# Optimization experiments

Hardware: AMD Instinct MI355X
Metric: run time of the kernel (lower is better)

## Reference

```python
import jax, jax.numpy as jnp
import numpy as np

B, D, H, S = 32768, 512, 8, 3  # batch, stream_dim, heads, num_streams
DH = D // H
EPS = 1e-5


def setup_inputs() -> dict:
    key = jax.random.key(0)
    ks = jax.random.split(key, 16)
    sc = lambda fan_in: 1.0 / np.sqrt(fan_in)
    return {
        "kinematic_h": jax.random.normal(ks[0], (B, D), jnp.float32),
        "color_h": jax.random.normal(ks[1], (B, D), jnp.float32),
        "spinor_h": jax.random.normal(ks[2], (B, D), jnp.float32),
        # MultiheadAttention packed in-proj and out-proj
        "w_in": jax.random.normal(ks[3], (3 * D, D), jnp.float32) * sc(D),
        "b_in": jnp.zeros((3 * D,), jnp.float32),
        "w_out": jax.random.normal(ks[4], (D, D), jnp.float32) * sc(D),
        "b_out": jnp.zeros((D,), jnp.float32),
        # stream gate: Linear(3D -> 3) + softmax
        "w_gate": jax.random.normal(ks[5], (S, S * D), jnp.float32) * sc(S * D),
        "b_gate": jnp.zeros((S,), jnp.float32),
        # fusion MLP: Linear(3D -> 2D), SiLU, Linear(2D -> D)
        "w1": jax.random.normal(ks[6], (2 * D, S * D), jnp.float32) * sc(S * D),
        "b1": jnp.zeros((2 * D,), jnp.float32),
        "w2": jax.random.normal(ks[7], (D, 2 * D), jnp.float32) * sc(2 * D),
        "b2": jnp.zeros((D,), jnp.float32),
        # LayerNorm
        "gamma": jnp.ones((D,), jnp.float32),
        "beta": jnp.zeros((D,), jnp.float32),
    }


def reference(kinematic_h, color_h, spinor_h, w_in, b_in, w_out, b_out,
              w_gate, b_gate, w1, b1, w2, b2, gamma, beta):
    stacked = jnp.stack([kinematic_h, color_h, spinor_h], axis=1)  # [B,S,D]
    b = stacked.shape[0]
    # self-attention (Q=K=V=stacked), packed QKV projection
    qkv = stacked @ w_in.T + b_in  # [B,S,3D]
    q, k, v = jnp.split(qkv, 3, axis=-1)
    q = q.reshape(b, S, H, DH)
    k = k.reshape(b, S, H, DH)
    v = v.reshape(b, S, H, DH)
    scores = jnp.einsum("bqhd,bkhd->bhqk", q, k) / np.sqrt(DH)
    attn = jax.nn.softmax(scores, axis=-1)
    out = jnp.einsum("bhqk,bkhd->bqhd", attn, v).reshape(b, S, D)
    attn_out = stacked + (out @ w_out.T + b_out)  # residual, [B,S,D]
    # gating softmax over streams
    flat = attn_out.reshape(b, S * D)
    gates = jax.nn.softmax(flat @ w_gate.T + b_gate, axis=-1)[..., None]  # [B,S,1]
    gated = (attn_out * gates).reshape(b, S * D)
    # fusion MLP (dropout=eval no-op)
    h = jax.nn.silu(gated @ w1.T + b1)
    fused = h @ w2.T + b2  # [B,D]
    # LayerNorm
    mu = jnp.mean(fused, axis=-1, keepdims=True)
    var = jnp.var(fused, axis=-1, keepdims=True)
    return (fused - mu) * jax.lax.rsqrt(var + EPS) * gamma + beta
```

## Files before the change

kernel.cpp:

```cpp
#include <hip/hip_runtime.h>
#include <stdint.h>


typedef float f32x4 __attribute__((ext_vector_type(4)));
typedef short bf16x8 __attribute__((ext_vector_type(8)));

__device__ __forceinline__ float bf2f(unsigned short h) {
  return __uint_as_float(((unsigned)h) << 16);
}
__device__ __forceinline__ unsigned short f2bf(float f) {
  unsigned u = __float_as_uint(f);
  u += 0x7FFFu + ((u >> 16) & 1u);
  return (unsigned short)(u >> 16);
}
__device__ __forceinline__ ushort4 f2bf4(float4 v) {
  return make_ushort4(f2bf(v.x), f2bf(v.y), f2bf(v.z), f2bf(v.w));
}

__device__ __forceinline__ void async_cp16(const void* g, void* lds) {
  __builtin_amdgcn_global_load_lds(
      (const __attribute__((address_space(1))) void*)g,
      (__attribute__((address_space(3))) void*)lds, 16, 0, 0);
}

__global__ void __launch_bounds__(256) cvtbf(const float4* __restrict__ src,
                                             ushort4* __restrict__ dst, int n4) {
  int i = blockIdx.x * 256 + threadIdx.x;
  if (i < n4) dst[i] = f2bf4(src[i]);
}

__global__ void __launch_bounds__(256) pack3(const float4* __restrict__ X0,
                                             const float4* __restrict__ X1,
                                             const float4* __restrict__ X2,
                                             ushort4* __restrict__ S) {
  int tid = blockIdx.x * 256 + threadIdx.x;
  int b = tid >> 7, c = tid & 127;
  long base = (long)(3 * b) * 128 + c;
  S[base]       = f2bf4(X0[tid]);
  S[base + 128] = f2bf4(X1[tid]);
  S[base + 256] = f2bf4(X2[tid]);
}

__global__ void __launch_bounds__(256)
qkv_attn(const unsigned short* __restrict__ S,
         const unsigned short* __restrict__ Wi,
         const float* __restrict__ bin,
         unsigned short* __restrict__ AO) {
  __shared__ unsigned short lds[96 * 200];
  unsigned short* Abuf = lds;
  unsigned short* Bbuf = lds + 6144;

  const int t = threadIdx.x;
  const int lane = t & 63;
  const int wave = t >> 6;
  const int wm = wave >> 1, wn = wave & 1;

  const int ny = gridDim.y;
  const int id = blockIdx.y * 8 + blockIdx.x;
  const int xcd = id & 7, j = id >> 3;
  const int h = j & 7;
  const long m0 = (long)(xcd * (ny >> 3) + (j >> 3)) * 96;

  const int trow = t >> 3;
  const int swz = ((t & 7) ^ (trow & 7)) << 3;
  const unsigned short* Ag = S + (m0 + trow) * 512 + swz;
  const unsigned short* Bg = Wi + ((long)h * 64 + trow) * 512 + swz;
  unsigned short* AsD = Abuf + t * 8;
  unsigned short* BsD = Bbuf + t * 8;

  f32x4 acc[3][6] = {};
  const int arow0 = wm * 48 + (lane & 15);
  const int brow0 = wn * 96 + (lane & 15);

  for (int k0 = 0; k0 < 512; k0 += 64) {
    __syncthreads();
#pragma unroll
    for (int r = 0; r < 3; r++)
      async_cp16(Ag + (long)r * 32 * 512 + k0, AsD + r * 2048);
#pragma unroll
    for (int r = 0; r < 6; r++)
      async_cp16(Bg + (long)((r >> 1) * 512 + (r & 1) * 32) * 512 + k0, BsD + r * 2048);
    __syncthreads();
#pragma unroll
    for (int kk = 0; kk < 2; kk++) {
      const int sc = ((kk * 4 + (lane >> 4)) ^ (lane & 7)) << 3;
      bf16x8 af[3], bfr[6];
#pragma unroll
      for (int mt = 0; mt < 3; mt++)
        af[mt] = *(const bf16x8*)&Abuf[(arow0 + mt * 16) * 64 + sc];
#pragma unroll
      for (int nt = 0; nt < 6; nt++)
        bfr[nt] = *(const bf16x8*)&Bbuf[(brow0 + nt * 16) * 64 + sc];
#pragma unroll
      for (int mt = 0; mt < 3; mt++)
#pragma unroll
        for (int nt = 0; nt < 6; nt++)
          acc[mt][nt] = __builtin_amdgcn_mfma_f32_16x16x32_bf16(
              af[mt], bfr[nt], acc[mt][nt], 0, 0, 0);
    }
  }

  __syncthreads();
  const int crow0 = wm * 48 + ((lane >> 4) << 2);
  const int ccol0 = wn * 96 + (lane & 15);
#pragma unroll
  for (int nt = 0; nt < 6; nt++) {
    const int col = ccol0 + nt * 16;
    const float bv = bin[(col >> 6) * 512 + h * 64 + (col & 63)];
#pragma unroll
    for (int mt = 0; mt < 3; mt++)
#pragma unroll
      for (int r = 0; r < 4; r++)
        lds[(crow0 + mt * 16 + r) * 200 + col] = f2bf(acc[mt][nt][r] + bv);
  }
  __syncthreads();

  const int bi = lane >> 3;
  const int l8 = lane & 7;
  const int r0 = (wave * 8 + bi) * 3;
  float q[3][8], k[3][8], v[3][8];
#pragma unroll
  for (int s = 0; s < 3; s++) {
    const unsigned short* rowp = &lds[(r0 + s) * 200 + l8 * 8];
    uint4 qu = *(const uint4*)(rowp);
    uint4 ku = *(const uint4*)(rowp + 64);
    uint4 vu = *(const uint4*)(rowp + 128);
    const unsigned* qw = (const unsigned*)&qu;
    const unsigned* kw = (const unsigned*)&ku;
    const unsigned* vw = (const unsigned*)&vu;
#pragma unroll
    for (int jj = 0; jj < 4; jj++) {
      q[s][2 * jj]     = __uint_as_float(qw[jj] << 16);
      q[s][2 * jj + 1] = __uint_as_float(qw[jj] & 0xffff0000u);
      k[s][2 * jj]     = __uint_as_float(kw[jj] << 16);
      k[s][2 * jj + 1] = __uint_as_float(kw[jj] & 0xffff0000u);
      v[s][2 * jj]     = __uint_as_float(vw[jj] << 16);
      v[s][2 * jj + 1] = __uint_as_float(vw[jj] & 0xffff0000u);
    }
  }
  float p[3][3];
#pragma unroll
  for (int s = 0; s < 3; s++)
#pragma unroll
    for (int u = 0; u < 3; u++) {
      float d = 0.f;
#pragma unroll
      for (int e = 0; e < 8; e++) d = fmaf(q[s][e], k[u][e], d);
      p[s][u] = d;
    }
#pragma unroll
  for (int m = 1; m < 8; m <<= 1)
#pragma unroll
    for (int s = 0; s < 3; s++)
#pragma unroll
      for (int u = 0; u < 3; u++) p[s][u] += __shfl_xor(p[s][u], m, 64);

  unsigned short* ob = AO + (m0 + r0) * 512 + h * 64 + l8 * 8;
#pragma unroll
  for (int s = 0; s < 3; s++) {
    float a0 = p[s][0] * 0.125f, a1 = p[s][1] * 0.125f, a2 = p[s][2] * 0.125f;
    float mx = fmaxf(a0, fmaxf(a1, a2));
    float e0 = __expf(a0 - mx), e1 = __expf(a1 - mx), e2 = __expf(a2 - mx);
    float inv = 1.0f / (e0 + e1 + e2);
    unsigned ow[4];
#pragma unroll
    for (int jj = 0; jj < 4; jj++) {
      float lo = (e0 * v[0][2 * jj] + e1 * v[1][2 * jj] + e2 * v[2][2 * jj]) * inv;
      float hi = (e0 * v[0][2 * jj + 1] + e1 * v[1][2 * jj + 1] + e2 * v[2][2 * jj + 1]) * inv;
      ow[jj] = (unsigned)f2bf(lo) | ((unsigned)f2bf(hi) << 16);
    }
    *(uint4*)(ob + s * 512) = *(uint4*)ow;
  }
}

enum { EPI_BF16 = 0, EPI_RES = 1, EPI_SILU = 2, EPI_F32 = 3 };

template <int EPI>
__global__ void __launch_bounds__(512, 2)
gemm256(const unsigned short* __restrict__ A,
        const unsigned short* __restrict__ W,
        const float* __restrict__ bias,
        const unsigned short* __restrict__ Res,
        void* __restrict__ Out,
        int K, int N) {
  __shared__ unsigned short As[2][16384];
  __shared__ unsigned short Bs[2][16384];
  const int t = threadIdx.x;
  const int lane = t & 63;
  const int wave = t >> 6;
  const int wm = wave >> 2, wn = wave & 3;

  const int nb = gridDim.x;
  const int nblocks = nb * gridDim.y;
  const int id = blockIdx.y * nb + blockIdx.x;
  const int lid = ((nblocks & 7) == 0) ? ((id & 7) * (nblocks >> 3) + (id >> 3)) : id;
  const long bm = (long)(lid / nb) * 256;
  const long bn = (long)(lid % nb) * 256;

  const int srow = t >> 3;
  const int sch = ((t & 7) ^ (srow & 7)) << 3;
  const unsigned short* Ag = A + (bm + srow) * (long)K + sch;
  const unsigned short* Wg = W + (bn + srow) * (long)K + sch;

  const int NT = K >> 6;

  f32x4 acc[8][4] = {};
  const int arow = wm * 128 + (lane & 15);
  const int brow = wn * 64 + (lane & 15);

#define STGA(buf, q, k0) \
  async_cp16(Ag + (long)((q) * 64) * K + (k0), &As[buf][(q) * 4096 + t * 8])
#define STGB(buf, q, k0) \
  async_cp16(Wg + (long)((q) * 64) * K + (k0), &Bs[buf][(q) * 4096 + t * 8])

  STGA(0, 0, 0); STGA(0, 2, 0);
  STGB(0, 0, 0); STGB(0, 1, 0); STGB(0, 2, 0); STGB(0, 3, 0);
  STGA(0, 1, 0); STGA(0, 3, 0);
  if (NT > 1) { STGA(1, 0, 64); STGA(1, 2, 64); }
  asm volatile("s_waitcnt vmcnt(0)" ::: "memory");
  __builtin_amdgcn_s_barrier();

  for (int tt = 0; tt < NT; ++tt) {
    const unsigned short* Ab = As[tt & 1];
    const unsigned short* Bb = Bs[tt & 1];
    const int nbuf = (tt & 1) ^ 1;
    const int k1 = (tt + 1) << 6, k2 = (tt + 2) << 6;
    const bool s1 = (tt + 1 < NT), s2 = (tt + 2 < NT);
    bf16x8 af[4], bfv[4];

    {
      const int sc = ((lane >> 4) ^ (lane & 7)) << 3;
#pragma unroll
      for (int i = 0; i < 4; ++i)
        af[i] = *(const bf16x8*)&Ab[(arow + i * 16) * 64 + sc];
#pragma unroll
      for (int i = 0; i < 4; ++i)
        bfv[i] = *(const bf16x8*)&Bb[(brow + i * 16) * 64 + sc];
      if (s1) { STGB(nbuf, 0, k1); STGB(nbuf, 1, k1); }
      __builtin_amdgcn_s_barrier();
      asm volatile("s_waitcnt lgkmcnt(0)" ::: "memory");
      __builtin_amdgcn_s_setprio(1);
#pragma unroll
      for (int mi = 0; mi < 4; ++mi)
#pragma unroll
        for (int ni = 0; ni < 4; ++ni)
          acc[mi][ni] = __builtin_amdgcn_mfma_f32_16x16x32_bf16(
              af[mi], bfv[ni], acc[mi][ni], 0, 0, 0);
      __builtin_amdgcn_s_setprio(0);
      asm volatile("s_waitcnt vmcnt(4)" ::: "memory");
      __builtin_amdgcn_s_barrier();
    }
    {
      const int sc = ((lane >> 4) ^ (lane & 7)) << 3;
#pragma unroll
      for (int i = 0; i < 4; ++i)
        af[i] = *(const bf16x8*)&Ab[(arow + (4 + i) * 16) * 64 + sc];
      if (s1) { STGB(nbuf, 2, k1); STGB(nbuf, 3, k1); }
      __builtin_amdgcn_s_barrier();
      asm volatile("s_waitcnt lgkmcnt(0)" ::: "memory");
      __builtin_amdgcn_s_setprio(1);
#pragma unroll
      for (int mi = 0; mi < 4; ++mi)
#pragma unroll
        for (int ni = 0; ni < 4; ++ni)
          acc[4 + mi][ni] = __builtin_amdgcn_mfma_f32_16x16x32_bf16(
              af[mi], bfv[ni], acc[4 + mi][ni], 0, 0, 0);
      __builtin_amdgcn_s_setprio(0);
      __builtin_amdgcn_s_barrier();
    }
    {
      const int sc = ((4 + (lane >> 4)) ^ (lane & 7)) << 3;
#pragma unroll
      for (int i = 0; i < 4; ++i)
        af[i] = *(const bf16x8*)&Ab[(arow + i * 16) * 64 + sc];
#pragma unroll
      for (int i = 0; i < 4; ++i)
        bfv[i] = *(const bf16x8*)&Bb[(brow + i * 16) * 64 + sc];
      if (s1) { STGA(nbuf, 1, k1); STGA(nbuf, 3, k1); }
      __builtin_amdgcn_s_barrier();
      asm volatile("s_waitcnt lgkmcnt(0)" ::: "memory");
      __builtin_amdgcn_s_setprio(1);
#pragma unroll
      for (int mi = 0; mi < 4; ++mi)
#pragma unroll
        for (int ni = 0; ni < 4; ++ni)
          acc[mi][ni] = __builtin_amdgcn_mfma_f32_16x16x32_bf16(
              af[mi], bfv[ni], acc[mi][ni], 0, 0, 0);
      __builtin_amdgcn_s_setprio(0);
      __builtin_amdgcn_s_barrier();
    }
    {
      const int sc = ((4 + (lane >> 4)) ^ (lane & 7)) << 3;
#pragma unroll
      for (int i = 0; i < 4; ++i)
        af[i] = *(const bf16x8*)&Ab[(arow + (4 + i) * 16) * 64 + sc];
      if (s2) { STGA(tt & 1, 0, k2); STGA(tt & 1, 2, k2); }
      __builtin_amdgcn_s_barrier();
      asm volatile("s_waitcnt lgkmcnt(0)" ::: "memory");
      __builtin_amdgcn_s_setprio(1);
#pragma unroll
      for (int mi = 0; mi < 4; ++mi)
#pragma unroll
        for (int ni = 0; ni < 4; ++ni)
          acc[4 + mi][ni] = __builtin_amdgcn_mfma_f32_16x16x32_bf16(
              af[mi], bfv[ni], acc[4 + mi][ni], 0, 0, 0);
      __builtin_amdgcn_s_setprio(0);
      asm volatile("s_waitcnt vmcnt(4)" ::: "memory");
      __builtin_amdgcn_s_barrier();
    }
  }
#undef STGA
#undef STGB

  const long row0 = bm + wm * 128 + ((lane >> 4) << 2);
  const int col0 = (int)bn + wn * 64 + (lane & 15);
#pragma unroll
  for (int nt = 0; nt < 4; ++nt) {
    const int col = col0 + nt * 16;
    const float bv = bias[col];
#pragma unroll
    for (int mt = 0; mt < 8; ++mt) {
      const long rbase = row0 + mt * 16;
#pragma unroll
      for (int r = 0; r < 4; ++r) {
        float v = acc[mt][nt][r] + bv;
        const long idx = (rbase + r) * (long)N + col;
        if (EPI == EPI_RES) v += bf2f(Res[idx]);
        if (EPI == EPI_SILU) v = v * (1.0f / (1.0f + __expf(-v)));
        if (EPI == EPI_F32)
          ((float*)Out)[idx] = v;
        else
          ((unsigned short*)Out)[idx] = f2bf(v);
      }
    }
  }
}

__global__ void __launch_bounds__(256) gate3(const unsigned short* AT,
                                             const float* __restrict__ WG,
                                             const float* __restrict__ BG,
                                             unsigned short* G) {
  int row = blockIdx.x * 4 + (threadIdx.x >> 6);
  int lane = threadIdx.x & 63;
  const unsigned short* rp = AT + (long)row * 1536 + lane * 8;
  float x[3][8];
  float p[3] = {0.f, 0.f, 0.f};
#pragma unroll
  for (int seg = 0; seg < 3; seg++) {
    uint4 u = *(const uint4*)(rp + seg * 512);
    const unsigned* uw = (const unsigned*)&u;
#pragma unroll
    for (int j = 0; j < 4; j++) {
      x[seg][2 * j]     = __uint_as_float(uw[j] << 16);
      x[seg][2 * j + 1] = __uint_as_float(uw[j] & 0xffff0000u);
    }
    const int e0 = seg * 512 + lane * 8;
#pragma unroll
    for (int g = 0; g < 3; g++) {
      const float* wp = WG + g * 1536 + e0;
#pragma unroll
      for (int e = 0; e < 8; e++) p[g] = fmaf(x[seg][e], wp[e], p[g]);
    }
  }
#pragma unroll
  for (int m = 1; m < 64; m <<= 1)
#pragma unroll
    for (int g = 0; g < 3; g++) p[g] += __shfl_xor(p[g], m, 64);
  float g0 = p[0] + BG[0], g1 = p[1] + BG[1], g2 = p[2] + BG[2];
  float mx = fmaxf(g0, fmaxf(g1, g2));
  g0 = __expf(g0 - mx); g1 = __expf(g1 - mx); g2 = __expf(g2 - mx);
  float inv = 1.0f / (g0 + g1 + g2);
  float gs[3] = {g0 * inv, g1 * inv, g2 * inv};
  unsigned short* op = G + (long)row * 1536 + lane * 8;
#pragma unroll
  for (int seg = 0; seg < 3; seg++) {
    unsigned ow[4];
#pragma unroll
    for (int j = 0; j < 4; j++)
      ow[j] = (unsigned)f2bf(x[seg][2 * j] * gs[seg]) |
              ((unsigned)f2bf(x[seg][2 * j + 1] * gs[seg]) << 16);
    *(uint4*)(op + seg * 512) = *(uint4*)ow;
  }
}

__global__ void __launch_bounds__(256) lnorm(const float* __restrict__ F,
                                             const float* __restrict__ gamma,
                                             const float* __restrict__ beta,
                                             float* __restrict__ out) {
  int row = blockIdx.x * 4 + (threadIdx.x >> 6);
  int lane = threadIdx.x & 63;
  const float4* fr = (const float4*)(F + (long)row * 512);
  float4 a = fr[lane], c = fr[lane + 64];
  float s = a.x + a.y + a.z + a.w + c.x + c.y + c.z + c.w;
  float ss = a.x * a.x + a.y * a.y + a.z * a.z + a.w * a.w +
             c.x * c.x + c.y * c.y + c.z * c.z + c.w * c.w;
#pragma unroll
  for (int m = 1; m < 64; m <<= 1) {
    s += __shfl_xor(s, m, 64);
    ss += __shfl_xor(ss, m, 64);
  }
  float mean = s * (1.0f / 512.0f);
  float var = ss * (1.0f / 512.0f) - mean * mean;
  float rstd = rsqrtf(var + 1e-5f);
  const float4* g4 = (const float4*)gamma;
  const float4* b4 = (const float4*)beta;
  float4 g0 = g4[lane], g1 = g4[lane + 64], be0 = b4[lane], be1 = b4[lane + 64];
  float4 o0, o1;
  o0.x = (a.x - mean) * rstd * g0.x + be0.x;
  o0.y = (a.y - mean) * rstd * g0.y + be0.y;
  o0.z = (a.z - mean) * rstd * g0.z + be0.z;
  o0.w = (a.w - mean) * rstd * g0.w + be0.w;
  o1.x = (c.x - mean) * rstd * g1.x + be1.x;
  o1.y = (c.y - mean) * rstd * g1.y + be1.y;
  o1.z = (c.z - mean) * rstd * g1.z + be1.z;
  o1.w = (c.w - mean) * rstd * g1.w + be1.w;
  float4* orow = (float4*)(out + (long)row * 512);
  orow[lane] = o0;
  orow[lane + 64] = o1;
}

extern "C" void kernel_launch(void* const* d_in, const int* in_sizes, int n_in,
                              void* d_out, int out_size, void* d_ws, size_t ws_size,
                              hipStream_t stream) {
  const float* kin    = (const float*)d_in[0];
  const float* colr   = (const float*)d_in[1];
  const float* spi    = (const float*)d_in[2];
  const float* w_in   = (const float*)d_in[3];
  const float* b_in   = (const float*)d_in[4];
  const float* w_out  = (const float*)d_in[5];
  const float* b_out  = (const float*)d_in[6];
  const float* w_gate = (const float*)d_in[7];
  const float* b_gate = (const float*)d_in[8];
  const float* w1     = (const float*)d_in[9];
  const float* b1     = (const float*)d_in[10];
  const float* w2     = (const float*)d_in[11];
  const float* b2     = (const float*)d_in[12];
  const float* gamma  = (const float*)d_in[13];
  const float* beta   = (const float*)d_in[14];
  float* out = (float*)d_out;

  long Bc = 32768;
  while (Bc > 1024 && (size_t)(6291456 + 9216 * Bc) > ws_size) Bc >>= 1;
  const int nch = (int)(32768 / Bc);

  char* ws = (char*)d_ws;
  unsigned short* Wic = (unsigned short*)(ws);
  unsigned short* Woc = (unsigned short*)(ws + 1572864);
  unsigned short* W1c = (unsigned short*)(ws + 2097152);
  unsigned short* W2c = (unsigned short*)(ws + 5242880);
  char* Sb  = ws + 6291456;
  char* AOb = Sb + 3072 * Bc;
  char* ATb = AOb + 3072 * Bc;

  cvtbf<<<768, 256, 0, stream>>>((const float4*)w_in, (ushort4*)Wic, 196608);
  cvtbf<<<256, 256, 0, stream>>>((const float4*)w_out, (ushort4*)Woc, 65536);
  cvtbf<<<1536, 256, 0, stream>>>((const float4*)w1, (ushort4*)W1c, 393216);
  cvtbf<<<512, 256, 0, stream>>>((const float4*)w2, (ushort4*)W2c, 131072);

  for (int c = 0; c < nch; c++) {
    const long boff = (long)c * Bc;
    unsigned short* S_c  = (unsigned short*)Sb;
    unsigned short* AO_c = (unsigned short*)AOb;
    unsigned short* AT_c = (unsigned short*)ATb;
    unsigned short* G_c  = AT_c;
    unsigned short* H_c  = (unsigned short*)AOb;
    float*          F_c  = (float*)Sb;

    pack3<<<(int)(Bc / 2), 256, 0, stream>>>(
        (const float4*)(kin + boff * 512), (const float4*)(colr + boff * 512),
        (const float4*)(spi + boff * 512), (ushort4*)S_c);
    qkv_attn<<<dim3(8, (int)(Bc / 32)), 256, 0, stream>>>(S_c, Wic, b_in, AO_c);
    gemm256<EPI_RES><<<dim3(2, (int)(3 * Bc / 256)), 512, 0, stream>>>(
        AO_c, Woc, b_out, S_c, AT_c, 512, 512);
    gate3<<<(int)(Bc / 4), 256, 0, stream>>>(AT_c, w_gate, b_gate, G_c);
    gemm256<EPI_SILU><<<dim3(4, (int)(Bc / 256)), 512, 0, stream>>>(
        G_c, W1c, b1, nullptr, H_c, 1536, 1024);
    gemm256<EPI_F32><<<dim3(2, (int)(Bc / 256)), 512, 0, stream>>>(
        H_c, W2c, b2, nullptr, F_c, 1024, 512);
    lnorm<<<(int)(Bc / 4), 256, 0, stream>>>(F_c, gamma, beta, out + boff * 512);
  }
}
```

Baseline: 841.6 us.

## Replace pipelined 256x256 GEMM with simple 128x128 single-buffer GEMM, packed bf16 converts

Swaps the hand-scheduled double-buffered 256x256-tile GEMM (512 threads, prefetch interleaved with MFMA phases, setprio) for a simpler 128x128-tile kernel with 256 threads, a single LDS buffer and barriers around each K step. The grids are rescaled to match. Separately, the bf16 conversion helpers now use the HIP packed float2-to-bf16x2 intrinsic in every kernel. The smaller tile gives more blocks and lower LDS and register use, but it loses load/compute overlap and halves operand reuse per tile, so the GEMMs may become latency-bound.

```diff
diff --git a/kernel.cpp b/kernel.cpp
--- a/kernel.cpp
+++ b/kernel.cpp
@@ -1,4 +1,5 @@
 #include <hip/hip_runtime.h>
+#include <hip/hip_bf16.h>
 #include <stdint.h>
 
 
@@ -9,12 +10,15 @@
   return __uint_as_float(((unsigned)h) << 16);
 }
 __device__ __forceinline__ unsigned short f2bf(float f) {
-  unsigned u = __float_as_uint(f);
-  u += 0x7FFFu + ((u >> 16) & 1u);
-  return (unsigned short)(u >> 16);
-}
-__device__ __forceinline__ ushort4 f2bf4(float4 v) {
-  return make_ushort4(f2bf(v.x), f2bf(v.y), f2bf(v.z), f2bf(v.w));
+  __hip_bfloat16 h = __float2bfloat16(f);
+  return *reinterpret_cast<unsigned short*>(&h);
+}
+__device__ __forceinline__ unsigned pack2bf(float lo, float hi) {
+  __hip_bfloat162 h2 = __float22bfloat162_rn(make_float2(lo, hi));
+  return *reinterpret_cast<unsigned*>(&h2);
+}
+__device__ __forceinline__ uint2 f2bf4p(float4 v) {
+  return make_uint2(pack2bf(v.x, v.y), pack2bf(v.z, v.w));
 }
 
 __device__ __forceinline__ void async_cp16(const void* g, void* lds) {
@@ -24,21 +28,21 @@
 }
 
 __global__ void __launch_bounds__(256) cvtbf(const float4* __restrict__ src,
-                                             ushort4* __restrict__ dst, int n4) {
+                                             uint2* __restrict__ dst, int n4) {
   int i = blockIdx.x * 256 + threadIdx.x;
-  if (i < n4) dst[i] = f2bf4(src[i]);
+  if (i < n4) dst[i] = f2bf4p(src[i]);
 }
 
 __global__ void __launch_bounds__(256) pack3(const float4* __restrict__ X0,
                                              const float4* __restrict__ X1,
                                              const float4* __restrict__ X2,
-                                             ushort4* __restrict__ S) {
+                                             uint2* __restrict__ S) {
   int tid = blockIdx.x * 256 + threadIdx.x;
   int b = tid >> 7, c = tid & 127;
   long base = (long)(3 * b) * 128 + c;
-  S[base]       = f2bf4(X0[tid]);
-  S[base + 128] = f2bf4(X1[tid]);
-  S[base + 256] = f2bf4(X2[tid]);
+  S[base]       = f2bf4p(X0[tid]);
+  S[base + 128] = f2bf4p(X1[tid]);
+  S[base + 256] = f2bf4p(X2[tid]);
 }
 
 __global__ void __launch_bounds__(256)
@@ -108,10 +112,15 @@
     const int col = ccol0 + nt * 16;
     const float bv = bin[(col >> 6) * 512 + h * 64 + (col & 63)];
 #pragma unroll
-    for (int mt = 0; mt < 3; mt++)
-#pragma unroll
-      for (int r = 0; r < 4; r++)
-        lds[(crow0 + mt * 16 + r) * 200 + col] = f2bf(acc[mt][nt][r] + bv);
+    for (int mt = 0; mt < 3; mt++) {
+      const int rb = (crow0 + mt * 16) * 200 + col;
+      const unsigned p01 = pack2bf(acc[mt][nt][0] + bv, acc[mt][nt][1] + bv);
+      const unsigned p23 = pack2bf(acc[mt][nt][2] + bv, acc[mt][nt][3] + bv);
+      lds[rb]       = (unsigned short)p01;
+      lds[rb + 200] = (unsigned short)(p01 >> 16);
+      lds[rb + 400] = (unsigned short)p23;
+      lds[rb + 600] = (unsigned short)(p23 >> 16);
+    }
   }
   __syncthreads();
 
@@ -167,7 +176,7 @@
     for (int jj = 0; jj < 4; jj++) {
       float lo = (e0 * v[0][2 * jj] + e1 * v[1][2 * jj] + e2 * v[2][2 * jj]) * inv;
       float hi = (e0 * v[0][2 * jj + 1] + e1 * v[1][2 * jj + 1] + e2 * v[2][2 * jj + 1]) * inv;
-      ow[jj] = (unsigned)f2bf(lo) | ((unsigned)f2bf(hi) << 16);
+      ow[jj] = pack2bf(lo, hi);
     }
     *(uint4*)(ob + s * 512) = *(uint4*)ow;
   }
@@ -176,153 +185,76 @@
 enum { EPI_BF16 = 0, EPI_RES = 1, EPI_SILU = 2, EPI_F32 = 3 };
 
 template <int EPI>
-__global__ void __launch_bounds__(512, 2)
-gemm256(const unsigned short* __restrict__ A,
+__global__ void __launch_bounds__(256)
+gemm_bt(const unsigned short* __restrict__ A,
         const unsigned short* __restrict__ W,
         const float* __restrict__ bias,
         const unsigned short* __restrict__ Res,
         void* __restrict__ Out,
         int K, int N) {
-  __shared__ unsigned short As[2][16384];
-  __shared__ unsigned short Bs[2][16384];
+  __shared__ unsigned short As[128 * 64];
+  __shared__ unsigned short Bs[128 * 64];
   const int t = threadIdx.x;
   const int lane = t & 63;
   const int wave = t >> 6;
-  const int wm = wave >> 2, wn = wave & 3;
+  const int wm = wave >> 1, wn = wave & 1;
 
   const int nb = gridDim.x;
   const int nblocks = nb * gridDim.y;
   const int id = blockIdx.y * nb + blockIdx.x;
   const int lid = ((nblocks & 7) == 0) ? ((id & 7) * (nblocks >> 3) + (id >> 3)) : id;
-  const long bm = (long)(lid / nb) * 256;
-  const long bn = (long)(lid % nb) * 256;
+  const long bm = (long)(lid / nb) * 128;
+  const long bn = (long)(lid % nb) * 128;
 
   const int srow = t >> 3;
-  const int sch = ((t & 7) ^ (srow & 7)) << 3;
-  const unsigned short* Ag = A + (bm + srow) * (long)K + sch;
-  const unsigned short* Wg = W + (bn + srow) * (long)K + sch;
-
-  const int NT = K >> 6;
-
-  f32x4 acc[8][4] = {};
-  const int arow = wm * 128 + (lane & 15);
-  const int brow = wn * 64 + (lane & 15);
-
-#define STGA(buf, q, k0) \
-  async_cp16(Ag + (long)((q) * 64) * K + (k0), &As[buf][(q) * 4096 + t * 8])
-#define STGB(buf, q, k0) \
-  async_cp16(Wg + (long)((q) * 64) * K + (k0), &Bs[buf][(q) * 4096 + t * 8])
-
-  STGA(0, 0, 0); STGA(0, 2, 0);
-  STGB(0, 0, 0); STGB(0, 1, 0); STGB(0, 2, 0); STGB(0, 3, 0);
-  STGA(0, 1, 0); STGA(0, 3, 0);
-  if (NT > 1) { STGA(1, 0, 64); STGA(1, 2, 64); }
-  asm volatile("s_waitcnt vmcnt(0)" ::: "memory");
-  __builtin_amdgcn_s_barrier();
-
-  for (int tt = 0; tt < NT; ++tt) {
-    const unsigned short* Ab = As[tt & 1];
-    const unsigned short* Bb = Bs[tt & 1];
-    const int nbuf = (tt & 1) ^ 1;
-    const int k1 = (tt + 1) << 6, k2 = (tt + 2) << 6;
-    const bool s1 = (tt + 1 < NT), s2 = (tt + 2 < NT);
-    bf16x8 af[4], bfv[4];
-
-    {
-      const int sc = ((lane >> 4) ^ (lane & 7)) << 3;
-#pragma unroll
-      for (int i = 0; i < 4; ++i)
-        af[i] = *(const bf16x8*)&Ab[(arow + i * 16) * 64 + sc];
-#pragma unroll
-      for (int i = 0; i < 4; ++i)
-        bfv[i] = *(const bf16x8*)&Bb[(brow + i * 16) * 64 + sc];
-      if (s1) { STGB(nbuf, 0, k1); STGB(nbuf, 1, k1); }
-      __builtin_amdgcn_s_barrier();
-      asm volatile("s_waitcnt lgkmcnt(0)" ::: "memory");
-      __builtin_amdgcn_s_setprio(1);
-#pragma unroll
-      for (int mi = 0; mi < 4; ++mi)
-#pragma unroll
-        for (int ni = 0; ni < 4; ++ni)
-          acc[mi][ni] = __builtin_amdgcn_mfma_f32_16x16x32_bf16(
-              af[mi], bfv[ni], acc[mi][ni], 0, 0, 0);
-      __builtin_amdgcn_s_setprio(0);
-      asm volatile("s_waitcnt vmcnt(4)" ::: "memory");
-      __builtin_amdgcn_s_barrier();
-    }
-    {
-      const int sc = ((lane >> 4) ^ (lane & 7)) << 3;
-#pragma unroll
-      for (int i = 0; i < 4; ++i)
-        af[i] = *(const bf16x8*)&Ab[(arow + (4 + i) * 16) * 64 + sc];
-      if (s1) { STGB(nbuf, 2, k1); STGB(nbuf, 3, k1); }
-      __builtin_amdgcn_s_barrier();
-      asm volatile("s_waitcnt lgkmcnt(0)" ::: "memory");
-      __builtin_amdgcn_s_setprio(1);
-#pragma unroll
-      for (int mi = 0; mi < 4; ++mi)
-#pragma unroll
-        for (int ni = 0; ni < 4; ++ni)
-          acc[4 + mi][ni] = __builtin_amdgcn_mfma_f32_16x16x32_bf16(
-              af[mi], bfv[ni], acc[4 + mi][ni], 0, 0, 0);
-      __builtin_amdgcn_s_setprio(0);
-      __builtin_amdgcn_s_barrier();
-    }
-    {
-      const int sc = ((4 + (lane >> 4)) ^ (lane & 7)) << 3;
-#pragma unroll
-      for (int i = 0; i < 4; ++i)
-        af[i] = *(const bf16x8*)&Ab[(arow + i * 16) * 64 + sc];
-#pragma unroll
-      for (int i = 0; i < 4; ++i)
-        bfv[i] = *(const bf16x8*)&Bb[(brow + i * 16) * 64 + sc];
-      if (s1) { STGA(nbuf, 1, k1); STGA(nbuf, 3, k1); }
-      __builtin_amdgcn_s_barrier();
-      asm volatile("s_waitcnt lgkmcnt(0)" ::: "memory");
-      __builtin_amdgcn_s_setprio(1);
-#pragma unroll
-      for (int mi = 0; mi < 4; ++mi)
-#pragma unroll
-        for (int ni = 0; ni < 4; ++ni)
-          acc[mi][ni] = __builtin_amdgcn_mfma_f32_16x16x32_bf16(
-              af[mi], bfv[ni], acc[mi][ni], 0, 0, 0);
-      __builtin_amdgcn_s_setprio(0);
-      __builtin_amdgcn_s_barrier();
-    }
-    {
-      const int sc = ((4 + (lane >> 4)) ^ (lane & 7)) << 3;
-#pragma unroll
-      for (int i = 0; i < 4; ++i)
-        af[i] = *(const bf16x8*)&Ab[(arow + (4 + i) * 16) * 64 + sc];
-      if (s2) { STGA(tt & 1, 0, k2); STGA(tt & 1, 2, k2); }
-      __builtin_amdgcn_s_barrier();
-      asm volatile("s_waitcnt lgkmcnt(0)" ::: "memory");
-      __builtin_amdgcn_s_setprio(1);
-#pragma unroll
-      for (int mi = 0; mi < 4; ++mi)
-#pragma unroll
-        for (int ni = 0; ni < 4; ++ni)
-          acc[4 + mi][ni] = __builtin_amdgcn_mfma_f32_16x16x32_bf16(
-              af[mi], bfv[ni], acc[4 + mi][ni], 0, 0, 0);
-      __builtin_amdgcn_s_setprio(0);
-      asm volatile("s_waitcnt vmcnt(4)" ::: "memory");
-      __builtin_amdgcn_s_barrier();
-    }
-  }
-#undef STGA
-#undef STGB
-
-  const long row0 = bm + wm * 128 + ((lane >> 4) << 2);
+  const int schunk = ((t & 7) ^ (srow & 7)) << 3;
+  const unsigned short* Ag = A + (bm + srow) * (long)K + schunk;
+  const unsigned short* Wg = W + (bn + srow) * (long)K + schunk;
+  unsigned short* AsD = As + t * 8;
+  unsigned short* BsD = Bs + t * 8;
+
+  f32x4 acc[4][4] = {};
+  const int arow0 = wm * 64 + (lane & 15);
+  const int brow0 = wn * 64 + (lane & 15);
+
+  for (int k0 = 0; k0 < K; k0 += 64) {
+    __syncthreads();
+#pragma unroll
+    for (int i = 0; i < 4; i++) {
+      async_cp16(Ag + (long)(i * 32) * K + k0, AsD + i * 2048);
+      async_cp16(Wg + (long)(i * 32) * K + k0, BsD + i * 2048);
+    }
+    __syncthreads();
+#pragma unroll
+    for (int kk = 0; kk < 2; kk++) {
+      const int sc = ((kk * 4 + (lane >> 4)) ^ (lane & 7)) << 3;
+      bf16x8 af[4], bfr[4];
+#pragma unroll
+      for (int mt = 0; mt < 4; mt++)
+        af[mt] = *(const bf16x8*)&As[(arow0 + mt * 16) * 64 + sc];
+#pragma unroll
+      for (int nt = 0; nt < 4; nt++)
+        bfr[nt] = *(const bf16x8*)&Bs[(brow0 + nt * 16) * 64 + sc];
+#pragma unroll
+      for (int mt = 0; mt < 4; mt++)
+#pragma unroll
+        for (int nt = 0; nt < 4; nt++)
+          acc[mt][nt] = __builtin_amdgcn_mfma_f32_16x16x32_bf16(
+              af[mt], bfr[nt], acc[mt][nt], 0, 0, 0);
+    }
+  }
+
+  const long row0 = bm + wm * 64 + ((lane >> 4) << 2);
   const int col0 = (int)bn + wn * 64 + (lane & 15);
 #pragma unroll
-  for (int nt = 0; nt < 4; ++nt) {
+  for (int nt = 0; nt < 4; nt++) {
     const int col = col0 + nt * 16;
     const float bv = bias[col];
 #pragma unroll
-    for (int mt = 0; mt < 8; ++mt) {
+    for (int mt = 0; mt < 4; mt++) {
       const long rbase = row0 + mt * 16;
 #pragma unroll
-      for (int r = 0; r < 4; ++r) {
+      for (int r = 0; r < 4; r++) {
         float v = acc[mt][nt][r] + bv;
         const long idx = (rbase + r) * (long)N + col;
         if (EPI == EPI_RES) v += bf2f(Res[idx]);
@@ -377,8 +309,7 @@
     unsigned ow[4];
 #pragma unroll
     for (int j = 0; j < 4; j++)
-      ow[j] = (unsigned)f2bf(x[seg][2 * j] * gs[seg]) |
-              ((unsigned)f2bf(x[seg][2 * j + 1] * gs[seg]) << 16);
+      ow[j] = pack2bf(x[seg][2 * j] * gs[seg], x[seg][2 * j + 1] * gs[seg]);
     *(uint4*)(op + seg * 512) = *(uint4*)ow;
   }
 }
@@ -452,10 +383,10 @@
   char* AOb = Sb + 3072 * Bc;
   char* ATb = AOb + 3072 * Bc;
 
-  cvtbf<<<768, 256, 0, stream>>>((const float4*)w_in, (ushort4*)Wic, 196608);
-  cvtbf<<<256, 256, 0, stream>>>((const float4*)w_out, (ushort4*)Woc, 65536);
-  cvtbf<<<1536, 256, 0, stream>>>((const float4*)w1, (ushort4*)W1c, 393216);
-  cvtbf<<<512, 256, 0, stream>>>((const float4*)w2, (ushort4*)W2c, 131072);
+  cvtbf<<<768, 256, 0, stream>>>((const float4*)w_in, (uint2*)Wic, 196608);
+  cvtbf<<<256, 256, 0, stream>>>((const float4*)w_out, (uint2*)Woc, 65536);
+  cvtbf<<<1536, 256, 0, stream>>>((const float4*)w1, (uint2*)W1c, 393216);
+  cvtbf<<<512, 256, 0, stream>>>((const float4*)w2, (uint2*)W2c, 131072);
 
   for (int c = 0; c < nch; c++) {
     const long boff = (long)c * Bc;
@@ -468,14 +399,14 @@
 
     pack3<<<(int)(Bc / 2), 256, 0, stream>>>(
         (const float4*)(kin + boff * 512), (const float4*)(colr + boff * 512),
-        (const float4*)(spi + boff * 512), (ushort4*)S_c);
+        (const float4*)(spi + boff * 512), (uint2*)S_c);
     qkv_attn<<<dim3(8, (int)(Bc / 32)), 256, 0, stream>>>(S_c, Wic, b_in, AO_c);
-    gemm256<EPI_RES><<<dim3(2, (int)(3 * Bc / 256)), 512, 0, stream>>>(
+    gemm_bt<EPI_RES><<<dim3(4, (int)(3 * Bc / 128)), 256, 0, stream>>>(
         AO_c, Woc, b_out, S_c, AT_c, 512, 512);
     gate3<<<(int)(Bc / 4), 256, 0, stream>>>(AT_c, w_gate, b_gate, G_c);
-    gemm256<EPI_SILU><<<dim3(4, (int)(Bc / 256)), 512, 0, stream>>>(
+    gemm_bt<EPI_SILU><<<dim3(8, (int)(Bc / 128)), 256, 0, stream>>>(
         G_c, W1c, b1, nullptr, H_c, 1536, 1024);
-    gemm256<EPI_F32><<<dim3(2, (int)(Bc / 256)), 512, 0, stream>>>(
+    gemm_bt<EPI_F32><<<dim3(4, (int)(Bc / 128)), 256, 0, stream>>>(
         H_c, W2c, b2, nullptr, F_c, 1024, 512);
     lnorm<<<(int)(Bc / 4), 256, 0, stream>>>(F_c, gamma, beta, out + boff * 512);
   }
```

After: 777.9 us. -7.6%, faster.
